# Optimization experiments

Measured on AMD Instinct MI355X. Metric: run time of the kernel, lower is better.

## Reference

```python
import jax, jax.numpy as jnp
import numpy as np

BATCH = 16384
NUM_IN = 4096
NUM_OUT = 1024
NNZ = 262144
BN_EPS = 1e-3  # keras BatchNormalization default epsilon


def setup_inputs() -> dict:
    key = jax.random.key(0)
    ks = jax.random.split(key, 6)
    x = jax.random.normal(ks[0], (BATCH, NUM_IN), dtype=jnp.float32)
    sp_values = jax.random.normal(ks[1], (NNZ,), dtype=jnp.float32)
    gamma = jnp.ones((NUM_IN,), dtype=jnp.float32)
    beta = jnp.zeros((NUM_IN,), dtype=jnp.float32)
    moving_mean = jax.random.normal(ks[2], (NUM_IN,), dtype=jnp.float32)
    # positive moving variance in [0.5, 1.5)
    moving_var = jax.random.uniform(ks[3], (NUM_IN,), dtype=jnp.float32, minval=0.5, maxval=1.5)
    sp_rows = jax.random.randint(ks[4], (NNZ,), 0, NUM_IN, dtype=jnp.int32)
    sp_cols = jax.random.randint(ks[5], (NNZ,), 0, NUM_OUT, dtype=jnp.int32)
    return {
        "x": x,
        "sp_values": sp_values,
        "gamma": gamma,
        "beta": beta,
        "moving_mean": moving_mean,
        "moving_var": moving_var,
        "sp_rows": sp_rows,
        "sp_cols": sp_cols,
    }


def reference(x, sp_values, gamma, beta, moving_mean, moving_var, sp_rows, sp_cols):
    # BatchNorm (inference mode, moving statistics), fused elementwise
    h = (x - moving_mean) * (gamma * jax.lax.rsqrt(moving_var + BN_EPS)) + beta
    # Scatter the fixed-index sparse weights into a small dense [NUM_IN, NUM_OUT]
    # matrix (16 MB), then a single dense GEMM — honors SparseTensor semantics
    # (duplicate indices accumulate) while staying GEMM-efficient.
    W = jnp.zeros((NUM_IN, NUM_OUT), dtype=x.dtype).at[sp_rows, sp_cols].add(sp_values)
    return h @ W  # [BATCH, NUM_OUT]
```

## Files before the change

kernel.cpp:

```cpp
#include <hip/hip_runtime.h>
#include <hip/hip_bf16.h>

#define BATCH   16384
#define NUM_IN  4096
#define NUM_OUT 1024
#define NNZ     262144
#define BN_EPS  1e-3f

typedef __attribute__((ext_vector_type(8)))  short short8;
typedef __attribute__((ext_vector_type(4)))  float f32x4;
typedef __attribute__((ext_vector_type(16))) float f32x16;
typedef __attribute__((ext_vector_type(4)))  unsigned int u32x4;

typedef __attribute__((address_space(3))) void        lds_void_t;
typedef const __attribute__((address_space(1))) void  g_void_t;

__device__ inline unsigned short f2bf(float f) {
    unsigned int u = __builtin_bit_cast(unsigned int, f);
    u += 0x7fffu + ((u >> 16) & 1u);
    return (unsigned short)(u >> 16);
}

__global__ void k_zero(f32x4* __restrict__ p) {
    p[(size_t)blockIdx.x * 256 + threadIdx.x] = f32x4{0.f, 0.f, 0.f, 0.f};
}

__global__ void k_scatter(const float* __restrict__ v, const int* __restrict__ r,
                          const int* __restrict__ c, float* __restrict__ wtf) {
    int i = blockIdx.x * 256 + threadIdx.x;
    atomicAdd(&wtf[(size_t)c[i] * NUM_IN + r[i]], v[i]);
}

__global__ void k_wprep(const float* __restrict__ wtf, const float* __restrict__ gamma,
                        const float* __restrict__ beta, const float* __restrict__ mean,
                        const float* __restrict__ var, unsigned short* __restrict__ wtb,
                        float* __restrict__ bias) {
    const int n = blockIdx.x;
    const int t = threadIdx.x;
    float acc = 0.f;
    for (int k = t; k < NUM_IN; k += 256) {
        float w = wtf[(size_t)n * NUM_IN + k];
        float s = gamma[k] * rsqrtf(var[k] + BN_EPS);
        wtb[(size_t)n * NUM_IN + k] = f2bf(w * s);
        acc += (beta[k] - mean[k] * s) * w;
    }
    #pragma unroll
    for (int o = 32; o; o >>= 1) acc += __shfl_down(acc, o, 64);
    __shared__ float red[4];
    if ((t & 63) == 0) red[t >> 6] = acc;
    __syncthreads();
    if (t == 0) bias[n] = red[0] + red[1] + red[2] + red[3];
}

#define BM 256
#define BN 256
#define BK 32
#define NT (NUM_IN / BK)
#define SLOT 32768
#define B_OFF 16384

__global__ __launch_bounds__(512, 2) void k_gemm(const float* __restrict__ x,
                                                 const unsigned short* __restrict__ wt,
                                                 const float* __restrict__ bias,
                                                 float* __restrict__ out) {
    __shared__ __align__(128) char lds[4 * SLOT];

    const int bid = blockIdx.x;
    const int swz = (bid & 7) * 32 + (bid >> 3);
    const int m0 = (swz >> 2) * BM;
    const int n0 = (swz & 3) * BN;

    const int t    = threadIdx.x;
    const int lane = t & 63;
    const int wid  = t >> 6;
    const int wm   = wid >> 2;
    const int wn   = wid & 3;

    const char* xb = (const char*)x;
    const char* wb = (const char*)wt;

    const int s_ar  = t >> 1;
    const int s_ah  = t & 1;
    const int a_swz = ((s_ar >> 1) & 3) << 4;
    const int s_bc  = t >> 2;
    const int s_bk  = (t & 3) * 16;

    f32x4 rA[2][4];

    auto stageB = [&](int kt, int slot) {
        #pragma unroll
        for (int i = 0; i < 2; ++i) {
            int c = i * 128 + s_bc;
            size_t src = (size_t)(n0 + c) * (NUM_IN * 2) + kt * (BK * 2)
                       + (s_bk ^ (((c >> 1) & 3) << 4));
            __builtin_amdgcn_global_load_lds((g_void_t*)(wb + src),
                (lds_void_t*)(lds + slot * SLOT + B_OFF + i * 8192 + t * 16), 16, 0, 0);
        }
    };
    auto loadA = [&](int kt, int rs) {
        size_t src = (size_t)(m0 + s_ar) * (NUM_IN * 4) + kt * (BK * 4) + s_ah * 64;
        #pragma unroll
        for (int j = 0; j < 4; ++j)
            rA[rs][j] = *(const f32x4*)(xb + src + j * 16);
    };
    auto writeA = [&](int slot, int rs) {
        const unsigned int* f = (const unsigned int*)&rA[rs][0];
        u32x4 p0, p1;
        p0[0] = __builtin_amdgcn_perm(f[1],  f[0],  0x07060302u);
        p0[1] = __builtin_amdgcn_perm(f[3],  f[2],  0x07060302u);
        p0[2] = __builtin_amdgcn_perm(f[5],  f[4],  0x07060302u);
        p0[3] = __builtin_amdgcn_perm(f[7],  f[6],  0x07060302u);
        p1[0] = __builtin_amdgcn_perm(f[9],  f[8],  0x07060302u);
        p1[1] = __builtin_amdgcn_perm(f[11], f[10], 0x07060302u);
        p1[2] = __builtin_amdgcn_perm(f[13], f[12], 0x07060302u);
        p1[3] = __builtin_amdgcn_perm(f[15], f[14], 0x07060302u);
        char* dst = lds + slot * SLOT + s_ar * 64;
        *(u32x4*)(dst + ((s_ah * 32 +  0) ^ a_swz)) = p0;
        *(u32x4*)(dst + ((s_ah * 32 + 16) ^ a_swz)) = p1;
    };

    const int fa_row = wm * 128 + (lane & 31);
    const int fb_col = wn * 64 + (lane & 31);
    const int f_kb   = (lane >> 5) * 16;

    short8 afr[4], bfr[2];
    auto readFrags = [&](int slot, int q) {
        const char* A = lds + slot * SLOT;
        const char* B = A + B_OFF;
        #pragma unroll
        for (int m = 0; m < 4; ++m) {
            int row = fa_row + m * 32;
            afr[m] = *(const short8*)(A + row * 64
                       + ((q * 32 + f_kb) ^ (((row >> 1) & 3) << 4)));
        }
        #pragma unroll
        for (int n = 0; n < 2; ++n) {
            int col = fb_col + n * 32;
            bfr[n] = *(const short8*)(B + col * 64
                       + ((q * 32 + f_kb) ^ (((col >> 1) & 3) << 4)));
        }
    };

    f32x16 acc[4][2] = {};
    auto domfma = [&]() {
        __builtin_amdgcn_s_setprio(1);
        #pragma unroll
        for (int m = 0; m < 4; ++m)
            #pragma unroll
            for (int n = 0; n < 2; ++n)
                acc[m][n] = __builtin_amdgcn_mfma_f32_32x32x16_bf16(
                    afr[m], bfr[n], acc[m][n], 0, 0, 0);
        __builtin_amdgcn_s_setprio(0);
    };

    auto body = [&](int kt, int rs, bool doStage, bool doConv, bool vm0) {
        const int cs = kt & 3;
        if (doStage) {
            stageB(kt + 2, (kt + 2) & 3);
            loadA(kt + 2, rs);
            __builtin_amdgcn_sched_barrier(0);
        }
        readFrags(cs, 0);
        asm volatile("s_waitcnt lgkmcnt(0)" ::: "memory");
        __builtin_amdgcn_sched_barrier(0);
        domfma();
        __builtin_amdgcn_s_barrier();
        readFrags(cs, 1);
        __builtin_amdgcn_sched_barrier(0);
        if (doConv) {
            if (vm0) asm volatile("s_waitcnt vmcnt(0)" ::: "memory");
            else     asm volatile("s_waitcnt vmcnt(6)" ::: "memory");
            writeA((kt + 1) & 3, rs ^ 1);
            asm volatile("s_waitcnt lgkmcnt(2)" ::: "memory");
        } else {
            asm volatile("s_waitcnt lgkmcnt(0)" ::: "memory");
        }
        __builtin_amdgcn_sched_barrier(0);
        domfma();
        asm volatile("s_waitcnt lgkmcnt(0)" ::: "memory");
        __builtin_amdgcn_s_barrier();
    };

    stageB(0, 0); loadA(0, 0);
    stageB(1, 1); loadA(1, 1);
    asm volatile("s_waitcnt vmcnt(6)" ::: "memory");
    writeA(0, 0);
    asm volatile("s_waitcnt lgkmcnt(0)" ::: "memory");
    __builtin_amdgcn_s_barrier();

    #pragma unroll 1
    for (int kt = 0; kt < NT - 2; kt += 2) {
        body(kt,     0, true, true, false);
        body(kt + 1, 1, true, true, false);
    }
    body(NT - 2, 0, false, true, true);
    body(NT - 1, 1, false, false, false);

    float bj[2];
    #pragma unroll
    for (int n = 0; n < 2; ++n) bj[n] = bias[n0 + wn * 64 + n * 32 + (lane & 31)];
    const int rbase = m0 + wm * 128 + 4 * (lane >> 5);
    const int cbase = n0 + wn * 64 + (lane & 31);
    #pragma unroll
    for (int m = 0; m < 4; ++m)
        #pragma unroll
        for (int n = 0; n < 2; ++n)
            #pragma unroll
            for (int r = 0; r < 16; ++r) {
                int row = rbase + m * 32 + (r & 3) + 8 * (r >> 2);
                out[(size_t)row * NUM_OUT + cbase + n * 32] = acc[m][n][r] + bj[n];
            }
}

extern "C" void kernel_launch(void* const* d_in, const int* in_sizes, int n_in,
                              void* d_out, int out_size, void* d_ws, size_t ws_size,
                              hipStream_t stream) {
    const float* x     = (const float*)d_in[0];
    const float* spv   = (const float*)d_in[1];
    const float* gamma = (const float*)d_in[2];
    const float* beta  = (const float*)d_in[3];
    const float* mean  = (const float*)d_in[4];
    const float* var   = (const float*)d_in[5];
    const int*   rows  = (const int*)d_in[6];
    const int*   cols  = (const int*)d_in[7];
    float* out = (float*)d_out;

    float* wtf = (float*)d_out;
    unsigned short* wtb = (unsigned short*)d_ws;
    float* bias = (float*)((char*)d_ws + (size_t)NUM_IN * NUM_OUT * sizeof(unsigned short));

    hipLaunchKernelGGL(k_zero, dim3((NUM_IN * NUM_OUT / 4) / 256), dim3(256), 0, stream,
                       (f32x4*)wtf);
    hipLaunchKernelGGL(k_scatter, dim3(NNZ / 256), dim3(256), 0, stream,
                       spv, rows, cols, wtf);
    hipLaunchKernelGGL(k_wprep, dim3(NUM_OUT), dim3(256), 0, stream,
                       wtf, gamma, beta, mean, var, wtb, bias);
    hipLaunchKernelGGL(k_gemm, dim3((BATCH / BM) * (NUM_OUT / BN)), dim3(512), 0, stream,
                       x, wtb, bias, out);
}
```

Before: 238.6 us.

## Restructure GEMM main loop to BK=64 double buffer with 16x16 MFMA

The GEMM mainloop changes from a four-slot BK=32 ring using 32x32x16 MFMAs to a two-slot BK=64 double buffer using 16x16x32 MFMAs. Each K tile is split into four MFMA phases, and the A loads, bf16 conversion and LDS writes are interleaved between those phases. The LDS swizzle is changed to a 128-byte row layout. This halves the number of K iterations and spreads memory work across the compute, but it adds many more barriers per tile. The 16x16 instruction also has lower fragment reuse per MFMA than the 32x32 one.

```diff
diff --git a/kernel.cpp b/kernel.cpp
--- a/kernel.cpp
+++ b/kernel.cpp
@@ -9,7 +9,6 @@
 
 typedef __attribute__((ext_vector_type(8)))  short short8;
 typedef __attribute__((ext_vector_type(4)))  float f32x4;
-typedef __attribute__((ext_vector_type(16))) float f32x16;
 typedef __attribute__((ext_vector_type(4)))  unsigned int u32x4;
 
 typedef __attribute__((address_space(3))) void        lds_void_t;
@@ -54,16 +53,16 @@
 
 #define BM 256
 #define BN 256
-#define BK 32
+#define BK 64
 #define NT (NUM_IN / BK)
-#define SLOT 32768
-#define B_OFF 16384
+#define SLOT 65536
+#define BOFF 32768
 
 __global__ __launch_bounds__(512, 2) void k_gemm(const float* __restrict__ x,
                                                  const unsigned short* __restrict__ wt,
                                                  const float* __restrict__ bias,
                                                  float* __restrict__ out) {
-    __shared__ __align__(128) char lds[4 * SLOT];
+    __shared__ __align__(128) char lds[2 * SLOT];
 
     const int bid = blockIdx.x;
     const int swz = (bid & 7) * 32 + (bid >> 3);
@@ -79,32 +78,38 @@
     const char* xb = (const char*)x;
     const char* wb = (const char*)wt;
 
-    const int s_ar  = t >> 1;
-    const int s_ah  = t & 1;
-    const int a_swz = ((s_ar >> 1) & 3) << 4;
-    const int s_bc  = t >> 2;
-    const int s_bk  = (t & 3) * 16;
-
-    f32x4 rA[2][4];
+    const int bg_r = t >> 3;
+    const int bg_c = (t & 7) * 16;
+    const int as_r = t & 255;
+    const int as_h = t >> 8;
+    const int as_s = (as_r & 7) << 4;
 
     auto stageB = [&](int kt, int slot) {
         #pragma unroll
-        for (int i = 0; i < 2; ++i) {
-            int c = i * 128 + s_bc;
-            size_t src = (size_t)(n0 + c) * (NUM_IN * 2) + kt * (BK * 2)
-                       + (s_bk ^ (((c >> 1) & 3) << 4));
+        for (int i = 0; i < 4; ++i) {
+            int row = i * 64 + bg_r;
+            size_t src = (size_t)(n0 + row) * (NUM_IN * 2) + (size_t)kt * (BK * 2)
+                       + (bg_c ^ ((row & 7) << 4));
             __builtin_amdgcn_global_load_lds((g_void_t*)(wb + src),
-                (lds_void_t*)(lds + slot * SLOT + B_OFF + i * 8192 + t * 16), 16, 0, 0);
+                (lds_void_t*)(lds + slot * SLOT + BOFF + i * 8192 + t * 16), 16, 0, 0);
         }
     };
-    auto loadA = [&](int kt, int rs) {
-        size_t src = (size_t)(m0 + s_ar) * (NUM_IN * 4) + kt * (BK * 4) + s_ah * 64;
-        #pragma unroll
-        for (int j = 0; j < 4; ++j)
-            rA[rs][j] = *(const f32x4*)(xb + src + j * 16);
-    };
-    auto writeA = [&](int slot, int rs) {
-        const unsigned int* f = (const unsigned int*)&rA[rs][0];
+
+    f32x4 rc0[4], rc1[4];
+    auto loadA0 = [&](int kt) {
+        size_t src = (size_t)(m0 + as_r) * (NUM_IN * 4) + (size_t)kt * (BK * 4)
+                   + as_h * 128;
+        #pragma unroll
+        for (int j = 0; j < 4; ++j) rc0[j] = *(const f32x4*)(xb + src + j * 16);
+    };
+    auto loadA1 = [&](int kt) {
+        size_t src = (size_t)(m0 + as_r) * (NUM_IN * 4) + (size_t)kt * (BK * 4)
+                   + as_h * 128 + 64;
+        #pragma unroll
+        for (int j = 0; j < 4; ++j) rc1[j] = *(const f32x4*)(xb + src + j * 16);
+    };
+    auto writeA = [&](int slot, const f32x4* rc, int qb) {
+        const unsigned int* f = (const unsigned int*)rc;
         u32x4 p0, p1;
         p0[0] = __builtin_amdgcn_perm(f[1],  f[0],  0x07060302u);
         p0[1] = __builtin_amdgcn_perm(f[3],  f[2],  0x07060302u);
@@ -114,102 +119,117 @@
         p1[1] = __builtin_amdgcn_perm(f[11], f[10], 0x07060302u);
         p1[2] = __builtin_amdgcn_perm(f[13], f[12], 0x07060302u);
         p1[3] = __builtin_amdgcn_perm(f[15], f[14], 0x07060302u);
-        char* dst = lds + slot * SLOT + s_ar * 64;
-        *(u32x4*)(dst + ((s_ah * 32 +  0) ^ a_swz)) = p0;
-        *(u32x4*)(dst + ((s_ah * 32 + 16) ^ a_swz)) = p1;
-    };
-
-    const int fa_row = wm * 128 + (lane & 31);
-    const int fb_col = wn * 64 + (lane & 31);
-    const int f_kb   = (lane >> 5) * 16;
-
-    short8 afr[4], bfr[2];
-    auto readFrags = [&](int slot, int q) {
+        char* dst = lds + slot * SLOT + as_r * 128;
+        *(u32x4*)(dst + ((as_h * 64 + qb * 16)      ^ as_s)) = p0;
+        *(u32x4*)(dst + ((as_h * 64 + qb * 16 + 16) ^ as_s)) = p1;
+    };
+
+    const int fa_r = wm * 128 + (lane & 15);
+    const int fb_r = wn * 64 + (lane & 15);
+    const int f_kb = (lane >> 4) * 16;
+
+    short8 bfr[4][2];
+    auto readB = [&](int slot) {
+        const char* B = lds + slot * SLOT + BOFF;
+        #pragma unroll
+        for (int j = 0; j < 4; ++j) {
+            int row = fb_r + j * 16;
+            int s = (row & 7) << 4;
+            #pragma unroll
+            for (int kk = 0; kk < 2; ++kk)
+                bfr[j][kk] = *(const short8*)(B + row * 128 + ((kk * 64 + f_kb) ^ s));
+        }
+    };
+    short8 af[2][2];
+    auto readA2 = [&](int slot, int p) {
         const char* A = lds + slot * SLOT;
-        const char* B = A + B_OFF;
-        #pragma unroll
-        for (int m = 0; m < 4; ++m) {
-            int row = fa_row + m * 32;
-            afr[m] = *(const short8*)(A + row * 64
-                       + ((q * 32 + f_kb) ^ (((row >> 1) & 3) << 4)));
+        #pragma unroll
+        for (int mi = 0; mi < 2; ++mi) {
+            int row = fa_r + (2 * p + mi) * 16;
+            int s = (row & 7) << 4;
+            #pragma unroll
+            for (int kk = 0; kk < 2; ++kk)
+                af[mi][kk] = *(const short8*)(A + row * 128 + ((kk * 64 + f_kb) ^ s));
         }
-        #pragma unroll
-        for (int n = 0; n < 2; ++n) {
-            int col = fb_col + n * 32;
-            bfr[n] = *(const short8*)(B + col * 64
-                       + ((q * 32 + f_kb) ^ (((col >> 1) & 3) << 4)));
-        }
-    };
-
-    f32x16 acc[4][2] = {};
-    auto domfma = [&]() {
+    };
+
+    f32x4 acc[8][4] = {};
+    auto mfma2 = [&](int p) {
         __builtin_amdgcn_s_setprio(1);
         #pragma unroll
-        for (int m = 0; m < 4; ++m)
-            #pragma unroll
-            for (int n = 0; n < 2; ++n)
-                acc[m][n] = __builtin_amdgcn_mfma_f32_32x32x16_bf16(
-                    afr[m], bfr[n], acc[m][n], 0, 0, 0);
+        for (int kk = 0; kk < 2; ++kk)
+            #pragma unroll
+            for (int mi = 0; mi < 2; ++mi)
+                #pragma unroll
+                for (int n = 0; n < 4; ++n)
+                    acc[2 * p + mi][n] = __builtin_amdgcn_mfma_f32_16x16x32_bf16(
+                        af[mi][kk], bfr[n][kk], acc[2 * p + mi][n], 0, 0, 0);
         __builtin_amdgcn_s_setprio(0);
     };
 
-    auto body = [&](int kt, int rs, bool doStage, bool doConv, bool vm0) {
-        const int cs = kt & 3;
-        if (doStage) {
-            stageB(kt + 2, (kt + 2) & 3);
-            loadA(kt + 2, rs);
-            __builtin_amdgcn_sched_barrier(0);
-        }
-        readFrags(cs, 0);
-        asm volatile("s_waitcnt lgkmcnt(0)" ::: "memory");
-        __builtin_amdgcn_sched_barrier(0);
-        domfma();
-        __builtin_amdgcn_s_barrier();
-        readFrags(cs, 1);
-        __builtin_amdgcn_sched_barrier(0);
-        if (doConv) {
-            if (vm0) asm volatile("s_waitcnt vmcnt(0)" ::: "memory");
-            else     asm volatile("s_waitcnt vmcnt(6)" ::: "memory");
-            writeA((kt + 1) & 3, rs ^ 1);
-            asm volatile("s_waitcnt lgkmcnt(2)" ::: "memory");
-        } else {
-            asm volatile("s_waitcnt lgkmcnt(0)" ::: "memory");
-        }
-        __builtin_amdgcn_sched_barrier(0);
-        domfma();
-        asm volatile("s_waitcnt lgkmcnt(0)" ::: "memory");
-        __builtin_amdgcn_s_barrier();
-    };
-
-    stageB(0, 0); loadA(0, 0);
-    stageB(1, 1); loadA(1, 1);
-    asm volatile("s_waitcnt vmcnt(6)" ::: "memory");
-    writeA(0, 0);
-    asm volatile("s_waitcnt lgkmcnt(0)" ::: "memory");
+    stageB(0, 0);
+    loadA0(0); loadA1(0);
+    writeA(0, rc0, 0);
+    writeA(0, rc1, 2);
+    asm volatile("s_waitcnt vmcnt(0) lgkmcnt(0)" ::: "memory");
     __builtin_amdgcn_s_barrier();
 
     #pragma unroll 1
-    for (int kt = 0; kt < NT - 2; kt += 2) {
-        body(kt,     0, true, true, false);
-        body(kt + 1, 1, true, true, false);
+    for (int kt = 0; kt < NT; ++kt) {
+        const int s = kt & 1;
+        const bool st = (kt + 1) < NT;
+        if (st) { stageB(kt + 1, s ^ 1); loadA0(kt + 1); }
+        readB(s); readA2(s, 0);
+        __builtin_amdgcn_sched_barrier(0);
+        __builtin_amdgcn_s_barrier();
+        asm volatile("s_waitcnt lgkmcnt(0)" ::: "memory");
+        __builtin_amdgcn_sched_barrier(0);
+        mfma2(0);
+        __builtin_amdgcn_sched_barrier(0);
+        __builtin_amdgcn_s_barrier();
+        if (st) loadA1(kt + 1);
+        readA2(s, 1);
+        __builtin_amdgcn_sched_barrier(0);
+        __builtin_amdgcn_s_barrier();
+        asm volatile("s_waitcnt lgkmcnt(0)" ::: "memory");
+        __builtin_amdgcn_sched_barrier(0);
+        mfma2(1);
+        __builtin_amdgcn_sched_barrier(0);
+        __builtin_amdgcn_s_barrier();
+        if (st) writeA(s ^ 1, rc0, 0);
+        readA2(s, 2);
+        __builtin_amdgcn_sched_barrier(0);
+        __builtin_amdgcn_s_barrier();
+        asm volatile("s_waitcnt lgkmcnt(0)" ::: "memory");
+        __builtin_amdgcn_sched_barrier(0);
+        mfma2(2);
+        __builtin_amdgcn_sched_barrier(0);
+        __builtin_amdgcn_s_barrier();
+        if (st) writeA(s ^ 1, rc1, 2);
+        readA2(s, 3);
+        if (st) asm volatile("s_waitcnt vmcnt(0)" ::: "memory");
+        __builtin_amdgcn_sched_barrier(0);
+        __builtin_amdgcn_s_barrier();
+        asm volatile("s_waitcnt lgkmcnt(0)" ::: "memory");
+        __builtin_amdgcn_sched_barrier(0);
+        mfma2(3);
+        __builtin_amdgcn_sched_barrier(0);
+        __builtin_amdgcn_s_barrier();
     }
-    body(NT - 2, 0, false, true, true);
-    body(NT - 1, 1, false, false, false);
-
-    float bj[2];
+
+    float bj[4];
     #pragma unroll
-    for (int n = 0; n < 2; ++n) bj[n] = bias[n0 + wn * 64 + n * 32 + (lane & 31)];
-    const int rbase = m0 + wm * 128 + 4 * (lane >> 5);
-    const int cbase = n0 + wn * 64 + (lane & 31);
+    for (int n = 0; n < 4; ++n) bj[n] = bias[n0 + wn * 64 + n * 16 + (lane & 15)];
+    const int mb = m0 + wm * 128 + (lane >> 4) * 4;
+    const int nb = n0 + wn * 64 + (lane & 15);
     #pragma unroll
-    for (int m = 0; m < 4; ++m)
-        #pragma unroll
-        for (int n = 0; n < 2; ++n)
-            #pragma unroll
-            for (int r = 0; r < 16; ++r) {
-                int row = rbase + m * 32 + (r & 3) + 8 * (r >> 2);
-                out[(size_t)row * NUM_OUT + cbase + n * 32] = acc[m][n][r] + bj[n];
-            }
+    for (int m = 0; m < 8; ++m)
+        #pragma unroll
+        for (int n = 0; n < 4; ++n)
+            #pragma unroll
+            for (int r = 0; r < 4; ++r)
+                out[(size_t)(mb + m * 16 + r) * NUM_OUT + (nb + n * 16)] =
+                    acc[m][n][r] + bj[n];
 }
 
 extern "C" void kernel_launch(void* const* d_in, const int* in_sizes, int n_in,
```

New measurement: 297.2 us. 24.5% more time.
